# Performance work log

Measured on AMD Instinct MI355X. Metric: run time of the kernel, lower is better.

## Reference

```python
import jax, jax.numpy as jnp
import numpy as np

C_MSA, C_PAIR, C, H = 64, 128, 32, 8
EPS = 1e-5


def _layernorm(x, w, b):
    mu = jnp.mean(x, axis=-1, keepdims=True)
    var = jnp.mean(jnp.square(x - mu), axis=-1, keepdims=True)
    return (x - mu) * jax.lax.rsqrt(var + EPS) * w + b


def setup_inputs() -> dict:
    key = jax.random.key(0)
    ks = jax.random.split(key, 8)
    B, S, N = 1, 512, 512
    msa = jax.random.normal(ks[0], (B, S, N, C_MSA), dtype=jnp.float32)
    pair = jax.random.normal(ks[1], (B, N, N, C_PAIR), dtype=jnp.float32)
    # LayerNorm params
    ln_msa_w = jnp.ones((C_MSA,), jnp.float32)
    ln_msa_b = jnp.zeros((C_MSA,), jnp.float32)
    ln_pair_w = jnp.ones((C_PAIR,), jnp.float32)
    ln_pair_b = jnp.zeros((C_PAIR,), jnp.float32)
    # Linear weights, [in, out] convention, no bias (LinearNoBias)
    sv = 1.0 / np.sqrt(C_MSA)
    sp = 1.0 / np.sqrt(C_PAIR)
    so = 1.0 / np.sqrt(C * H)
    Wv = jax.random.uniform(ks[2], (C_MSA, C * H), jnp.float32, -sv, sv)
    Wb = jax.random.uniform(ks[3], (C_PAIR, H), jnp.float32, -sp, sp)
    Wg = jax.random.uniform(ks[4], (C_MSA, C * H), jnp.float32, -sv, sv)
    Wo = jax.random.uniform(ks[5], (C * H, C_MSA), jnp.float32, -so, so)
    return {"msa": msa, "pair": pair, "ln_msa_w": ln_msa_w, "ln_msa_b": ln_msa_b,
            "ln_pair_w": ln_pair_w, "ln_pair_b": ln_pair_b,
            "Wv": Wv, "Wb": Wb, "Wg": Wg, "Wo": Wo}


def reference(msa, pair, ln_msa_w, ln_msa_b, ln_pair_w, ln_pair_b, Wv, Wb, Wg, Wo):
    B, S, N, _ = msa.shape
    mn = _layernorm(msa, ln_msa_w, ln_msa_b)            # [B,S,N,c_msa]
    pn = _layernorm(pair, ln_pair_w, ln_pair_b)         # [B,N,N,c_pair]
    v = (mn @ Wv).reshape(B, S, N, H, C)                # values per head
    g = jax.nn.sigmoid(mn @ Wg).reshape(B, S, N, H, C)  # gates
    b = pn @ Wb                                         # [B,i,j,H] pair bias
    w = jax.nn.softmax(b, axis=2)                       # softmax over j
    # shared attention weights applied to every MSA row s
    o = jnp.einsum('bijh,bsjhc->bsihc', w, v)
    o = (g * o).reshape(B, S, N, H * C)
    return o @ Wo                                        # [B,S,N,c_msa]
```

## Files before the change

kernel.cpp:

```cpp
#include <hip/hip_runtime.h>
#include <stdint.h>

typedef short bf16x8 __attribute__((ext_vector_type(8)));
typedef float f32x4 __attribute__((ext_vector_type(4)));
typedef unsigned long long u64;

__device__ __forceinline__ float bf2f(unsigned short u){
  union { unsigned int i; float f; } c; c.i = ((unsigned int)u) << 16; return c.f;
}
__device__ __forceinline__ unsigned short f2bf(float f){
  unsigned int x = __float_as_uint(f);
  return (unsigned short)((x + 0x7FFFu + ((x >> 16) & 1u)) >> 16);
}

union FragU { bf16x8 v; uint4 u; };

#define OFF_WVT 0ull
#define OFF_WGT 32768ull
#define OFF_WOT 65536ull
#define OFF_W   131072ull
#define OFF_VT  8388608ull
#define OFF_O   142606336ull

__global__ __launch_bounds__(256) void k0_weights(const float* __restrict__ Wv,
                                                  const float* __restrict__ Wg,
                                                  const float* __restrict__ Wo,
                                                  unsigned short* __restrict__ wvt,
                                                  unsigned short* __restrict__ wgt,
                                                  unsigned short* __restrict__ wot){
  int idx = blockIdx.x * 256 + threadIdx.x;
  if (idx < 16384){ int k = idx >> 8, n = idx & 255; wvt[n * 64 + k] = f2bf(Wv[idx]); }
  else if (idx < 32768){ int j = idx - 16384; int k = j >> 8, n = j & 255; wgt[n * 64 + k] = f2bf(Wg[j]); }
  else if (idx < 49152){ int j = idx - 32768; int k = j >> 6, n = j & 63;  wot[n * 256 + k] = f2bf(Wo[j]); }
}

__device__ __forceinline__ float fold8(float ph[8], int lane){
#pragma unroll
  for (int u = 0; u < 4; ++u){
    float snd = (lane & 1) ? ph[u] : ph[u + 4];
    float t = __shfl_xor(snd, 1);
    ph[u] = ((lane & 1) ? ph[u + 4] : ph[u]) + t;
  }
#pragma unroll
  for (int u = 0; u < 2; ++u){
    float snd = (lane & 2) ? ph[u] : ph[u + 2];
    float t = __shfl_xor(snd, 2);
    ph[u] = ((lane & 2) ? ph[u + 2] : ph[u]) + t;
  }
  {
    float snd = (lane & 4) ? ph[0] : ph[1];
    float t = __shfl_xor(snd, 4);
    ph[0] = ((lane & 4) ? ph[1] : ph[0]) + t;
  }
  ph[0] += __shfl_xor(ph[0], 8);
  ph[0] += __shfl_xor(ph[0], 16);
  ph[0] += __shfl_xor(ph[0], 32);
  return ph[0];
}

__global__ __launch_bounds__(256) void k1a_bias(const float* __restrict__ pair,
                                                const float* __restrict__ lnw,
                                                const float* __restrict__ lnb,
                                                const float* __restrict__ Wb,
                                                float* __restrict__ bbuf){
  __shared__ float bstage[32][9];
  const int tid = threadIdx.x, lane = tid & 63, wave = tid >> 6;
  const int r0 = blockIdx.x * 32;
  const int c0 = 2 * lane, c1 = 2 * lane + 1;
  float wb0[8], wb1[8];
#pragma unroll
  for (int h = 0; h < 8; ++h){ wb0[h] = Wb[c0 * 8 + h]; wb1[h] = Wb[c1 * 8 + h]; }
  const float lw0 = lnw[c0], lb0v = lnb[c0], lw1 = lnw[c1], lb1v = lnb[c1];
  const int hL = ((lane & 1) << 2) | (lane & 2) | ((lane >> 2) & 1);

#pragma unroll
  for (int it = 0; it < 4; ++it){
    const int rA = r0 + wave * 8 + it * 2;
    float2 xA = *(const float2*)(pair + (size_t)rA * 128 + c0);
    float2 xB = *(const float2*)(pair + ((size_t)rA + 1) * 128 + c0);
    float sA = xA.x + xA.y, qA = xA.x * xA.x + xA.y * xA.y;
    float sB = xB.x + xB.y, qB = xB.x * xB.x + xB.y * xB.y;
#pragma unroll
    for (int o = 1; o < 64; o <<= 1){
      sA += __shfl_xor(sA, o); qA += __shfl_xor(qA, o);
      sB += __shfl_xor(sB, o); qB += __shfl_xor(qB, o);
    }
    const float mA = sA * (1.f / 128.f), mB = sB * (1.f / 128.f);
    const float rsA = rsqrtf(qA * (1.f / 128.f) - mA * mA + 1e-5f);
    const float rsB = rsqrtf(qB * (1.f / 128.f) - mB * mB + 1e-5f);
    const float a0 = (xA.x - mA) * rsA * lw0 + lb0v;
    const float a1 = (xA.y - mA) * rsA * lw1 + lb1v;
    const float b0 = (xB.x - mB) * rsB * lw0 + lb0v;
    const float b1 = (xB.y - mB) * rsB * lw1 + lb1v;
    float phA[8], phB[8];
#pragma unroll
    for (int h = 0; h < 8; ++h){
      phA[h] = a0 * wb0[h] + a1 * wb1[h];
      phB[h] = b0 * wb0[h] + b1 * wb1[h];
    }
    float vA = fold8(phA, lane);
    float vB = fold8(phB, lane);
    if (lane < 8){
      bstage[wave * 8 + it * 2][hL]     = vA;
      bstage[wave * 8 + it * 2 + 1][hL] = vB;
    }
  }
  __syncthreads();
  {
    int h = tid >> 5, idx = tid & 31;
    bbuf[(size_t)h * 262144 + r0 + idx] = bstage[idx][h];
  }
}

__global__ __launch_bounds__(256) void k1b_softmax(const float* __restrict__ bbuf,
                                                   unsigned short* __restrict__ wout){
  const int tid = threadIdx.x, lane = tid & 63, wave = tid >> 6;
  const int row = blockIdx.x * 4 + wave;
  const float* src = bbuf + (size_t)row * 512;
  float4 v0 = *(const float4*)(src + lane * 8);
  float4 v1 = *(const float4*)(src + lane * 8 + 4);
  float e[8] = {v0.x, v0.y, v0.z, v0.w, v1.x, v1.y, v1.z, v1.w};
  float m = e[0];
#pragma unroll
  for (int t = 1; t < 8; ++t) m = fmaxf(m, e[t]);
#pragma unroll
  for (int o = 1; o < 64; o <<= 1) m = fmaxf(m, __shfl_xor(m, o));
  float sum = 0.f;
#pragma unroll
  for (int t = 0; t < 8; ++t){ e[t] = __expf(e[t] - m); sum += e[t]; }
#pragma unroll
  for (int o = 1; o < 64; o <<= 1) sum += __shfl_xor(sum, o);
  const float inv = 1.0f / sum;
  unsigned int pk[4];
#pragma unroll
  for (int u = 0; u < 4; ++u)
    pk[u] = (unsigned)f2bf(e[u * 2] * inv) | ((unsigned)f2bf(e[u * 2 + 1] * inv) << 16);
  *(uint4*)(wout + (size_t)row * 512 + lane * 8) = make_uint4(pk[0], pk[1], pk[2], pk[3]);
}

__global__ __launch_bounds__(256) void k2_v(const float* __restrict__ msa,
                                            const float* __restrict__ lnw,
                                            const float* __restrict__ lnb,
                                            const unsigned short* __restrict__ wvt,
                                            unsigned short* __restrict__ vt){
  __shared__ unsigned short smem[18432];
  __shared__ float lnw_s[64], lnb_s[64];
  const int tid = threadIdx.x, lane = tid & 63, wave = tid >> 6;
  const int bx = blockIdx.x;
  const int sIdx = bx >> 2, n0 = (bx & 3) * 128;
  const int cb = blockIdx.y * 128;
  const int g = lane >> 4, l15 = lane & 15;
  if (tid < 64){ lnw_s[tid] = lnw[tid]; lnb_s[tid] = lnb[tid]; }
  const int row = tid >> 1, half = tid & 1;
  float4 xv[8];
  {
    const float4* src = (const float4*)(msa + ((size_t)(sIdx * 512 + n0 + row)) * 64 + half * 32);
#pragma unroll
    for (int u = 0; u < 8; ++u) xv[u] = src[u];
  }
  {
    const uint4* src = (const uint4*)(wvt + (size_t)(cb + row) * 64 + half * 32);
    uint4* dst = (uint4*)&smem[9216 + row * 72 + half * 32];
#pragma unroll
    for (int u = 0; u < 4; ++u) dst[u] = src[u];
  }
  float sS = 0.f, qS = 0.f;
#pragma unroll
  for (int u = 0; u < 8; ++u){
    sS += xv[u].x + xv[u].y + xv[u].z + xv[u].w;
    qS += xv[u].x * xv[u].x + xv[u].y * xv[u].y + xv[u].z * xv[u].z + xv[u].w * xv[u].w;
  }
  sS += __shfl_xor(sS, 1); qS += __shfl_xor(qS, 1);
  const float mean = sS * (1.f / 64.f);
  const float var = qS * (1.f / 64.f) - mean * mean;
  const float rstd = rsqrtf(var + 1e-5f);
  __syncthreads();
  {
    unsigned int pk[16];
#pragma unroll
    for (int u = 0; u < 8; ++u){
      const int cbase = half * 32 + u * 4;
      float a0 = (xv[u].x - mean) * rstd * lnw_s[cbase + 0] + lnb_s[cbase + 0];
      float a1 = (xv[u].y - mean) * rstd * lnw_s[cbase + 1] + lnb_s[cbase + 1];
      float a2 = (xv[u].z - mean) * rstd * lnw_s[cbase + 2] + lnb_s[cbase + 2];
      float a3 = (xv[u].w - mean) * rstd * lnw_s[cbase + 3] + lnb_s[cbase + 3];
      pk[u * 2]     = (unsigned)f2bf(a0) | ((unsigned)f2bf(a1) << 16);
      pk[u * 2 + 1] = (unsigned)f2bf(a2) | ((unsigned)f2bf(a3) << 16);
    }
    uint4* dst = (uint4*)&smem[row * 72 + half * 32];
#pragma unroll
    for (int u = 0; u < 4; ++u) dst[u] = make_uint4(pk[u * 4], pk[u * 4 + 1], pk[u * 4 + 2], pk[u * 4 + 3]);
  }
  __syncthreads();
  const int wm = wave >> 1, wn = wave & 1;
  const f32x4 z = {0.f, 0.f, 0.f, 0.f};
  f32x4 acc[4][4];
#pragma unroll
  for (int a = 0; a < 4; ++a)
#pragma unroll
    for (int b = 0; b < 4; ++b) acc[a][b] = z;
#pragma unroll
  for (int kk = 0; kk < 64; kk += 32){
    bf16x8 av[4], bv[4];
#pragma unroll
    for (int mf = 0; mf < 4; ++mf){
      FragU f; f.u = *(const uint4*)&smem[(wm * 64 + mf * 16 + l15) * 72 + kk + 8 * g];
      av[mf] = f.v;
    }
#pragma unroll
    for (int nf = 0; nf < 4; ++nf){
      FragU f; f.u = *(const uint4*)&smem[9216 + (wn * 64 + nf * 16 + l15) * 72 + kk + 8 * g];
      bv[nf] = f.v;
    }
#pragma unroll
    for (int mf = 0; mf < 4; ++mf)
#pragma unroll
      for (int nf = 0; nf < 4; ++nf)
        acc[mf][nf] = __builtin_amdgcn_mfma_f32_16x16x32_bf16(av[mf], bv[nf], acc[mf][nf], 0, 0, 0);
  }
  __syncthreads();
#pragma unroll
  for (int nf = 0; nf < 4; ++nf){
    int hcL = wn * 64 + nf * 16 + l15;
#pragma unroll
    for (int mf = 0; mf < 4; ++mf){
      int nbase = wm * 64 + mf * 16 + 4 * g;
      u64 qv = (u64)f2bf(acc[mf][nf][0])
             | ((u64)f2bf(acc[mf][nf][1]) << 16)
             | ((u64)f2bf(acc[mf][nf][2]) << 32)
             | ((u64)f2bf(acc[mf][nf][3]) << 48);
      *(u64*)&smem[hcL * 136 + nbase] = qv;
    }
  }
  __syncthreads();
  {
    int hcL = tid >> 1, nh = tid & 1;
    int hc = cb + hcL;
    int hIdx = hc >> 5, c = hc & 31;
    unsigned short* dst = vt + ((size_t)(hIdx * 16384 + sIdx * 32 + c)) * 512 + n0 + nh * 64;
    const uint4* src = (const uint4*)&smem[hcL * 136 + nh * 64];
#pragma unroll
    for (int u = 0; u < 8; ++u) ((uint4*)dst)[u] = src[u];
  }
}

__global__ __launch_bounds__(256) void k3_attn(const unsigned short* __restrict__ wp,
                                               const unsigned short* __restrict__ vt,
                                               unsigned short* __restrict__ o){
  __shared__ unsigned short A_s[128 * 72];
  __shared__ unsigned short B_s[128 * 72];
  const int tid = threadIdx.x, lane = tid & 63, wave = tid >> 6;
  const int sc0 = blockIdx.x * 128, i0 = blockIdx.y * 128, h = blockIdx.z;
  const int wm = wave >> 1, wn = wave & 1;
  const int g = lane >> 4, l15 = lane & 15;
  const int srow = tid >> 1, shalf = tid & 1;
  const unsigned short* wbase = wp + ((size_t)(h * 512 + i0 + srow)) * 512 + shalf * 32;
  const unsigned short* vbase = vt + ((size_t)(h * 16384 + sc0 + srow)) * 512 + shalf * 32;
  const f32x4 z = {0.f, 0.f, 0.f, 0.f};
  f32x4 acc[4][4];
#pragma unroll
  for (int a = 0; a < 4; ++a)
#pragma unroll
    for (int b = 0; b < 4; ++b) acc[a][b] = z;

  for (int kt = 0; kt < 8; ++kt){
    const int j0 = kt * 64;
    __syncthreads();
    {
      const uint4* ga = (const uint4*)(wbase + j0);
      uint4* da = (uint4*)&A_s[srow * 72 + shalf * 32];
#pragma unroll
      for (int u = 0; u < 4; ++u) da[u] = ga[u];
      const uint4* gb = (const uint4*)(vbase + j0);
      uint4* db = (uint4*)&B_s[srow * 72 + shalf * 32];
#pragma unroll
      for (int u = 0; u < 4; ++u) db[u] = gb[u];
    }
    __syncthreads();
#pragma unroll
    for (int kk = 0; kk < 64; kk += 32){
      bf16x8 av[4], bv[4];
#pragma unroll
      for (int mf = 0; mf < 4; ++mf){
        FragU f; f.u = *(const uint4*)&A_s[(wm * 64 + mf * 16 + l15) * 72 + kk + 8 * g];
        av[mf] = f.v;
      }
#pragma unroll
      for (int nf = 0; nf < 4; ++nf){
        FragU f; f.u = *(const uint4*)&B_s[(wn * 64 + nf * 16 + l15) * 72 + kk + 8 * g];
        bv[nf] = f.v;
      }
#pragma unroll
      for (int mf = 0; mf < 4; ++mf)
#pragma unroll
        for (int nf = 0; nf < 4; ++nf)
          acc[mf][nf] = __builtin_amdgcn_mfma_f32_16x16x32_bf16(av[mf], bv[nf], acc[mf][nf], 0, 0, 0);
    }
  }
#pragma unroll
  for (int nf = 0; nf < 4; ++nf){
    int col_sc = sc0 + wn * 64 + nf * 16 + l15;
    int sIdx = col_sc >> 5, c = col_sc & 31;
#pragma unroll
    for (int mf = 0; mf < 4; ++mf){
      int rbase = i0 + wm * 64 + mf * 16 + 4 * g;
#pragma unroll
      for (int e = 0; e < 4; ++e)
        o[((size_t)(sIdx * 512 + rbase + e)) * 256 + h * 32 + c] = f2bf(acc[mf][nf][e]);
    }
  }
}

__global__ __launch_bounds__(256) void k4_out(const float* __restrict__ msa,
                                              const float* __restrict__ lnw,
                                              const float* __restrict__ lnb,
                                              const unsigned short* __restrict__ ot,
                                              const unsigned short* __restrict__ wgt,
                                              const unsigned short* __restrict__ wot,
                                              float* __restrict__ out){
  __shared__ unsigned short o_s[64 * 256];
  __shared__ unsigned short mnb[64 * 72];
  __shared__ unsigned short X_s[64 * 40];
  __shared__ unsigned short wg_s[32 * 72];
  __shared__ unsigned short wo_s[64 * 40];
  __shared__ float lnw_s[64], lnb_s[64];
  const int tid = threadIdx.x, lane = tid & 63, wave = tid >> 6;
  const int r0 = blockIdx.x * 64;
  const int g = lane >> 4, l15 = lane & 15;
  if (tid < 64){ lnw_s[tid] = lnw[tid]; lnb_s[tid] = lnb[tid]; }
  {
    int row = tid >> 2, q = tid & 3;
    const uint4* src = (const uint4*)(ot + ((size_t)(r0 + row)) * 256 + q * 64);
    uint4* dst = (uint4*)&o_s[row * 256 + q * 64];
#pragma unroll
    for (int u = 0; u < 8; ++u) dst[u] = src[u];
  }
  const int lrow = tid >> 2, lq = tid & 3;
  float4 xv[4];
  {
    const float4* src = (const float4*)(msa + ((size_t)(r0 + lrow)) * 64 + lq * 16);
#pragma unroll
    for (int u = 0; u < 4; ++u) xv[u] = src[u];
  }
  float sS = 0.f, qS = 0.f;
#pragma unroll
  for (int u = 0; u < 4; ++u){
    sS += xv[u].x + xv[u].y + xv[u].z + xv[u].w;
    qS += xv[u].x * xv[u].x + xv[u].y * xv[u].y + xv[u].z * xv[u].z + xv[u].w * xv[u].w;
  }
  sS += __shfl_xor(sS, 1); qS += __shfl_xor(qS, 1);
  sS += __shfl_xor(sS, 2); qS += __shfl_xor(qS, 2);
  const float mean = sS * (1.f / 64.f);
  const float var = qS * (1.f / 64.f) - mean * mean;
  const float rstd = rsqrtf(var + 1e-5f);
  __syncthreads();
  {
    unsigned int pk[8];
#pragma unroll
    for (int u = 0; u < 4; ++u){
      const int cbase = lq * 16 + u * 4;
      float a0 = (xv[u].x - mean) * rstd * lnw_s[cbase + 0] + lnb_s[cbase + 0];
      float a1 = (xv[u].y - mean) * rstd * lnw_s[cbase + 1] + lnb_s[cbase + 1];
      float a2 = (xv[u].z - mean) * rstd * lnw_s[cbase + 2] + lnb_s[cbase + 2];
      float a3 = (xv[u].w - mean) * rstd * lnw_s[cbase + 3] + lnb_s[cbase + 3];
      pk[u * 2]     = (unsigned)f2bf(a0) | ((unsigned)f2bf(a1) << 16);
      pk[u * 2 + 1] = (unsigned)f2bf(a2) | ((unsigned)f2bf(a3) << 16);
    }
    uint4* dst = (uint4*)&mnb[lrow * 72 + lq * 16];
    dst[0] = make_uint4(pk[0], pk[1], pk[2], pk[3]);
    dst[1] = make_uint4(pk[4], pk[5], pk[6], pk[7]);
  }
  const int wm = wave >> 1, wn = wave & 1;
  const f32x4 z = {0.f, 0.f, 0.f, 0.f};
  f32x4 accO[2][2];
  accO[0][0] = z; accO[0][1] = z; accO[1][0] = z; accO[1][1] = z;

  for (int h = 0; h < 8; ++h){
    __syncthreads();
    if (tid < 64){
      int row = tid >> 1, hf = tid & 1;
      const uint4* src = (const uint4*)(wgt + (size_t)(h * 32 + row) * 64 + hf * 32);
      uint4* dst = (uint4*)&wg_s[row * 72 + hf * 32];
#pragma unroll
      for (int u = 0; u < 4; ++u) dst[u] = src[u];
    } else if (tid < 192){
      int t = tid - 64; int row = t >> 1, hf = t & 1;
      const uint4* src = (const uint4*)(wot + (size_t)row * 256 + h * 32 + hf * 16);
      uint4* dst = (uint4*)&wo_s[row * 40 + hf * 16];
      dst[0] = src[0]; dst[1] = src[1];
    }
    __syncthreads();
    f32x4 gacc[2]; gacc[0] = z; gacc[1] = z;
#pragma unroll
    for (int kk = 0; kk < 64; kk += 32){
      FragU a; a.u = *(const uint4*)&mnb[(wave * 16 + l15) * 72 + kk + 8 * g];
#pragma unroll
      for (int nf = 0; nf < 2; ++nf){
        FragU b; b.u = *(const uint4*)&wg_s[(nf * 16 + l15) * 72 + kk + 8 * g];
        gacc[nf] = __builtin_amdgcn_mfma_f32_16x16x32_bf16(a.v, b.v, gacc[nf], 0, 0, 0);
      }
    }
#pragma unroll
    for (int nf = 0; nf < 2; ++nf){
#pragma unroll
      for (int e = 0; e < 4; ++e){
        int row = wave * 16 + 4 * g + e;
        int col = nf * 16 + l15;
        float gv = 1.0f / (1.0f + __expf(-gacc[nf][e]));
        float ov = bf2f(o_s[row * 256 + h * 32 + col]);
        X_s[row * 40 + col] = f2bf(gv * ov);
      }
    }
    __syncthreads();
#pragma unroll
    for (int mf = 0; mf < 2; ++mf){
      FragU a; a.u = *(const uint4*)&X_s[(wm * 32 + mf * 16 + l15) * 40 + 8 * g];
#pragma unroll
      for (int nf = 0; nf < 2; ++nf){
        FragU b; b.u = *(const uint4*)&wo_s[(wn * 32 + nf * 16 + l15) * 40 + 8 * g];
        accO[mf][nf] = __builtin_amdgcn_mfma_f32_16x16x32_bf16(a.v, b.v, accO[mf][nf], 0, 0, 0);
      }
    }
  }
#pragma unroll
  for (int mf = 0; mf < 2; ++mf)
#pragma unroll
    for (int nf = 0; nf < 2; ++nf)
#pragma unroll
      for (int e = 0; e < 4; ++e){
        int row = wm * 32 + mf * 16 + 4 * g + e;
        int col = wn * 32 + nf * 16 + l15;
        out[((size_t)(r0 + row)) * 64 + col] = accO[mf][nf][e];
      }
}

extern "C" void kernel_launch(void* const* d_in, const int* in_sizes, int n_in,
                              void* d_out, int out_size, void* d_ws, size_t ws_size,
                              hipStream_t stream){
  const float* msa       = (const float*)d_in[0];
  const float* pair      = (const float*)d_in[1];
  const float* ln_msa_w  = (const float*)d_in[2];
  const float* ln_msa_b  = (const float*)d_in[3];
  const float* ln_pair_w = (const float*)d_in[4];
  const float* ln_pair_b = (const float*)d_in[5];
  const float* Wv        = (const float*)d_in[6];
  const float* Wb        = (const float*)d_in[7];
  const float* Wg        = (const float*)d_in[8];
  const float* Wo        = (const float*)d_in[9];
  float* out = (float*)d_out;
  char* ws = (char*)d_ws;
  unsigned short* wvt = (unsigned short*)(ws + OFF_WVT);
  unsigned short* wgt = (unsigned short*)(ws + OFF_WGT);
  unsigned short* wot = (unsigned short*)(ws + OFF_WOT);
  unsigned short* wsm = (unsigned short*)(ws + OFF_W);
  unsigned short* vt  = (unsigned short*)(ws + OFF_VT);
  unsigned short* obuf= (unsigned short*)(ws + OFF_O);
  float* bbuf = (float*)(ws + OFF_VT);

  hipLaunchKernelGGL(k0_weights,  dim3(192),        dim3(256), 0, stream, Wv, Wg, Wo, wvt, wgt, wot);
  hipLaunchKernelGGL(k1a_bias,    dim3(8192),       dim3(256), 0, stream, pair, ln_pair_w, ln_pair_b, Wb, bbuf);
  hipLaunchKernelGGL(k1b_softmax, dim3(1024),       dim3(256), 0, stream, bbuf, wsm);
  hipLaunchKernelGGL(k2_v,        dim3(2048, 2),    dim3(256), 0, stream, msa, ln_msa_w, ln_msa_b, wvt, vt);
  hipLaunchKernelGGL(k3_attn,     dim3(128, 4, 8),  dim3(256), 0, stream, wsm, vt, obuf);
  hipLaunchKernelGGL(k4_out,      dim3(4096),       dim3(256), 0, stream, msa, ln_msa_w, ln_msa_b, obuf, wgt, wot, out);
}
```

Baseline: 387.7 us.

## Use direct global-to-LDS loads and stage attention output through LDS for coalesced stores

The attention GEMM kernel now fills its A and B tiles with global_load_lds instructions that write straight into shared memory without passing through registers. Because of this, the padded row stride of 72 is dropped and the tiles use an unpadded stride of 64. The epilogue first writes the bf16 results to a padded shared-memory tile and then stores them as 16-byte vectors, replacing the scattered 2-byte global stores. The unpadded layout may cause LDS bank conflicts when fragments are read, and the epilogue adds two barriers.

Measured after the change: 398.5 us. 2.8% more time.

```diff
diff --git a/kernel.cpp b/kernel.cpp
--- a/kernel.cpp
+++ b/kernel.cpp
@@ -14,6 +14,12 @@
 }
 
 union FragU { bf16x8 v; uint4 u; };
+
+__device__ __forceinline__ void gld16(const unsigned short* g, unsigned short* l){
+  __builtin_amdgcn_global_load_lds(
+      (const __attribute__((address_space(1))) void*)g,
+      (__attribute__((address_space(3))) void*)l, 16, 0, 0);
+}
 
 #define OFF_WVT 0ull
 #define OFF_WGT 32768ull
@@ -247,15 +253,17 @@
 __global__ __launch_bounds__(256) void k3_attn(const unsigned short* __restrict__ wp,
                                                const unsigned short* __restrict__ vt,
                                                unsigned short* __restrict__ o){
-  __shared__ unsigned short A_s[128 * 72];
-  __shared__ unsigned short B_s[128 * 72];
+  __shared__ unsigned short sm[17408];
   const int tid = threadIdx.x, lane = tid & 63, wave = tid >> 6;
   const int sc0 = blockIdx.x * 128, i0 = blockIdx.y * 128, h = blockIdx.z;
   const int wm = wave >> 1, wn = wave & 1;
   const int g = lane >> 4, l15 = lane & 15;
-  const int srow = tid >> 1, shalf = tid & 1;
-  const unsigned short* wbase = wp + ((size_t)(h * 512 + i0 + srow)) * 512 + shalf * 32;
-  const unsigned short* vbase = vt + ((size_t)(h * 16384 + sc0 + srow)) * 512 + shalf * 32;
+  const int ldRow = wave * 32 + (lane >> 3);
+  const int ldCol = (lane & 7) * 8;
+  const unsigned short* aSrc = wp + ((size_t)(h * 512 + i0 + ldRow)) * 512 + ldCol;
+  const unsigned short* bSrc = vt + ((size_t)(h * 16384 + sc0 + ldRow)) * 512 + ldCol;
+  unsigned short* aDst = &sm[wave * 2048];
+  unsigned short* bDst = &sm[8192 + wave * 2048];
   const f32x4 z = {0.f, 0.f, 0.f, 0.f};
   f32x4 acc[4][4];
 #pragma unroll
@@ -266,15 +274,10 @@
   for (int kt = 0; kt < 8; ++kt){
     const int j0 = kt * 64;
     __syncthreads();
-    {
-      const uint4* ga = (const uint4*)(wbase + j0);
-      uint4* da = (uint4*)&A_s[srow * 72 + shalf * 32];
-#pragma unroll
-      for (int u = 0; u < 4; ++u) da[u] = ga[u];
-      const uint4* gb = (const uint4*)(vbase + j0);
-      uint4* db = (uint4*)&B_s[srow * 72 + shalf * 32];
-#pragma unroll
-      for (int u = 0; u < 4; ++u) db[u] = gb[u];
+#pragma unroll
+    for (int q = 0; q < 4; ++q){
+      gld16(aSrc + q * 4096 + j0, aDst + q * 512);
+      gld16(bSrc + q * 4096 + j0, bDst + q * 512);
     }
     __syncthreads();
 #pragma unroll
@@ -282,12 +285,12 @@
       bf16x8 av[4], bv[4];
 #pragma unroll
       for (int mf = 0; mf < 4; ++mf){
-        FragU f; f.u = *(const uint4*)&A_s[(wm * 64 + mf * 16 + l15) * 72 + kk + 8 * g];
+        FragU f; f.u = *(const uint4*)&sm[(wm * 64 + mf * 16 + l15) * 64 + kk + 8 * g];
         av[mf] = f.v;
       }
 #pragma unroll
       for (int nf = 0; nf < 4; ++nf){
-        FragU f; f.u = *(const uint4*)&B_s[(wn * 64 + nf * 16 + l15) * 72 + kk + 8 * g];
+        FragU f; f.u = *(const uint4*)&sm[8192 + (wn * 64 + nf * 16 + l15) * 64 + kk + 8 * g];
         bv[nf] = f.v;
       }
 #pragma unroll
@@ -297,16 +300,32 @@
           acc[mf][nf] = __builtin_amdgcn_mfma_f32_16x16x32_bf16(av[mf], bv[nf], acc[mf][nf], 0, 0, 0);
     }
   }
-#pragma unroll
-  for (int nf = 0; nf < 4; ++nf){
-    int col_sc = sc0 + wn * 64 + nf * 16 + l15;
-    int sIdx = col_sc >> 5, c = col_sc & 31;
-#pragma unroll
-    for (int mf = 0; mf < 4; ++mf){
-      int rbase = i0 + wm * 64 + mf * 16 + 4 * g;
-#pragma unroll
-      for (int e = 0; e < 4; ++e)
-        o[((size_t)(sIdx * 512 + rbase + e)) * 256 + h * 32 + c] = f2bf(acc[mf][nf][e]);
+  __syncthreads();
+#pragma unroll
+  for (int mf = 0; mf < 4; ++mf){
+#pragma unroll
+    for (int nf = 0; nf < 4; ++nf){
+      int col = wn * 64 + nf * 16 + l15;
+#pragma unroll
+      for (int e = 0; e < 4; ++e){
+        int rowi = wm * 64 + mf * 16 + 4 * g + e;
+        sm[rowi * 136 + col] = f2bf(acc[mf][nf][e]);
+      }
+    }
+  }
+  __syncthreads();
+  {
+    const int il = tid >> 1, half = tid & 1;
+#pragma unroll
+    for (int grp = 0; grp < 2; ++grp){
+      int col0 = half * 64 + grp * 32;
+      int sIdx = (sc0 >> 5) + (col0 >> 5);
+      unsigned short* dst = o + ((size_t)(sIdx * 512 + i0 + il)) * 256 + h * 32;
+      const uint4* srcp = (const uint4*)&sm[il * 136 + col0];
+      ((uint4*)dst)[0] = srcp[0];
+      ((uint4*)dst)[1] = srcp[1];
+      ((uint4*)dst)[2] = srcp[2];
+      ((uint4*)dst)[3] = srcp[3];
     }
   }
 }
```
